# Performance work log

Hardware: AMD Instinct MI355X
Metric: run time of the kernel (lower is better)

## Reference

```python
import jax, jax.numpy as jnp
import numpy as np

N = 100000
E = 1600000
DIM = 64
HEADS = 8
HEAD_DIM = DIM // HEADS
LN_EPS = 1e-5
NORM_EPS = 1e-12


def setup_inputs() -> dict:
    key = jax.random.key(0)
    ks = jax.random.split(key, 5)
    x = jax.random.normal(ks[0], (N, DIM), dtype=jnp.float32)
    edge_index = jax.random.randint(ks[1], (2, E), 0, N, dtype=jnp.int32)
    W_w = jax.random.normal(ks[2], (DIM, DIM), dtype=jnp.float32) * (1.0 / np.sqrt(DIM))
    W_b = jax.random.normal(ks[3], (DIM,), dtype=jnp.float32) * 0.01
    a = jax.random.normal(ks[4], (HEADS, 2 * HEAD_DIM), dtype=jnp.float32) * 0.1
    ln_scale = jnp.ones((DIM,), dtype=jnp.float32)
    ln_bias = jnp.zeros((DIM,), dtype=jnp.float32)
    return {"x": x, "edge_index": edge_index, "W_w": W_w, "W_b": W_b,
            "a": a, "ln_scale": ln_scale, "ln_bias": ln_bias}


def reference(x, edge_index, W_w, W_b, a, ln_scale, ln_bias):
    n = x.shape[0]
    # Linear (dropout = identity in eval), reshape to heads
    h = (x @ W_w.T + W_b).reshape(n, HEADS, HEAD_DIM)          # [N,H,D]
    src, dst = edge_index[0], edge_index[1]
    hs = h[src]                                                 # [E,H,D]
    hd = h[dst]                                                 # [E,H,D]
    a_src, a_dst = a[:, :HEAD_DIM], a[:, HEAD_DIM:]             # [H,D] each
    # (a * cat(hs, hd)).sum(-1) split over the two halves
    alpha = jnp.einsum('ehd,hd->eh', hs, a_src) + jnp.einsum('ehd,hd->eh', hd, a_dst)
    alpha = jnp.where(alpha >= 0, alpha, 0.2 * alpha)           # LeakyReLU(0.2)
    alpha = jax.nn.softmax(alpha, axis=1)                       # NOTE: over heads, as in source
    msg = alpha[..., None] * hd                                 # [E,H,D]
    out = jax.ops.segment_sum(msg, src, num_segments=n)         # scatter-add to src nodes
    out = out.reshape(n, DIM)
    # residual + LayerNorm
    y = out + x
    mu = jnp.mean(y, axis=-1, keepdims=True)
    var = jnp.mean((y - mu) ** 2, axis=-1, keepdims=True)
    y = (y - mu) * jax.lax.rsqrt(var + LN_EPS) * ln_scale + ln_bias
    # F.normalize(p=2, dim=-1)
    norm = jnp.sqrt(jnp.sum(y * y, axis=-1, keepdims=True))
    return y / jnp.maximum(norm, NORM_EPS)
```

## Files before the change

kernel.cpp:

```cpp
#include <hip/hip_runtime.h>
#include <hip/hip_fp16.h>
#include <math.h>

#define N_NODES 100000
#define N_EDGES 1600000
#define LN_EPS 1e-5f
#define NORM_EPS 1e-12f
#define ROWS_PER_BLOCK 32
#define GEMM_BLOCKS (N_NODES / ROWS_PER_BLOCK)
#define WSTRIDE 66
#define WB 64
#define NBKT ((N_NODES + WB - 1) / WB)
#define BIN_TILE 8192
#define BIN_BLOCKS ((N_EDGES + BIN_TILE - 1) / BIN_TILE)

__global__ __launch_bounds__(256) void k_gemm(
    const float* __restrict__ x, const float* __restrict__ W,
    const float* __restrict__ b, const float* __restrict__ a,
    __half* __restrict__ h16,
    float* __restrict__ s_src, float* __restrict__ s_dst)
{
    __shared__ float WL[64 * WSTRIDE];
    __shared__ float xs[ROWS_PER_BLOCK * 64];
    const int tid  = threadIdx.x;
    const int lane = tid & 63;
    const int wv   = tid >> 6;

    for (int idx = tid * 4; idx < 64 * 64; idx += 256 * 4) {
        const float4 w = *(const float4*)(W + idx);
        const int c = idx >> 6, k = idx & 63;
        WL[c * WSTRIDE + k + 0] = w.x;
        WL[c * WSTRIDE + k + 1] = w.y;
        WL[c * WSTRIDE + k + 2] = w.z;
        WL[c * WSTRIDE + k + 3] = w.w;
    }
    const int row0 = blockIdx.x * ROWS_PER_BLOCK;
    for (int idx = tid * 4; idx < ROWS_PER_BLOCK * 64; idx += 256 * 4)
        *(float4*)(xs + idx) = *(const float4*)(x + (size_t)row0 * 64 + idx);
    __syncthreads();

    const float bias = b[lane];
    float acc[8];
    #pragma unroll
    for (int r = 0; r < 8; ++r) acc[r] = bias;

    const int rbase = wv * 8;
    const float* wrow = WL + lane * WSTRIDE;
    const float* xrow = xs + rbase * 64;
    #pragma unroll 1
    for (int kk = 0; kk < 64; kk += 4) {
        const float2 w01 = *(const float2*)(wrow + kk);
        const float2 w23 = *(const float2*)(wrow + kk + 2);
        #pragma unroll
        for (int r = 0; r < 8; ++r) {
            const float4 xq = *(const float4*)(xrow + r * 64 + kk);
            acc[r] += xq.x * w01.x + xq.y * w01.y + xq.z * w23.x + xq.w * w23.y;
        }
    }

    const float asrc = a[(lane >> 3) * 16 + (lane & 7)];
    const float adst = a[(lane >> 3) * 16 + 8 + (lane & 7)];
    #pragma unroll
    for (int r = 0; r < 8; ++r) {
        const int row = row0 + rbase + r;
        const float v = acc[r];
        h16[(size_t)row * 64 + lane] = __float2half_rn(v);
        float p = v * asrc, q = v * adst;
        p += __shfl_xor(p, 1);  q += __shfl_xor(q, 1);
        p += __shfl_xor(p, 2);  q += __shfl_xor(q, 2);
        p += __shfl_xor(p, 4);  q += __shfl_xor(q, 4);
        if ((lane & 7) == 0) {
            s_src[row * 8 + (lane >> 3)] = p;
            s_dst[row * 8 + (lane >> 3)] = q;
        }
    }
}

__global__ __launch_bounds__(1024) void k_hist(
    const int* __restrict__ ei, int* __restrict__ bhist)
{
    __shared__ int hist[NBKT];
    const int tid = threadIdx.x;
    for (int b = tid; b < NBKT; b += 1024) hist[b] = 0;
    __syncthreads();
    const int e0 = blockIdx.x * BIN_TILE;
    #pragma unroll
    for (int j = 0; j < 8; ++j) {
        const int e = e0 + j * 1024 + tid;
        if (e < N_EDGES) atomicAdd(&hist[ei[e] >> 6], 1);
    }
    __syncthreads();
    for (int b = tid; b < NBKT; b += 1024)
        if (hist[b]) atomicAdd(&bhist[b], hist[b]);
}

__global__ __launch_bounds__(1024) void k_bscan(
    const int* __restrict__ bhist, int* __restrict__ bucket_base,
    int* __restrict__ gbin)
{
    __shared__ int wsum[16];
    const int tid = threadIdx.x, lane = tid & 63, wv = tid >> 6;

    int v = (tid < NBKT) ? bhist[tid] : 0;
    int sc = v;
    #pragma unroll
    for (int off = 1; off < 64; off <<= 1) {
        int t = __shfl_up(sc, off);
        if (lane >= off) sc += t;
    }
    if (lane == 63) wsum[wv] = sc;
    __syncthreads();
    if (tid < 16) {
        int ws = wsum[tid];
        #pragma unroll
        for (int off = 1; off < 16; off <<= 1) {
            int t = __shfl_up(ws, off);
            if (tid >= off) ws += t;
        }
        wsum[tid] = ws;
    }
    __syncthreads();
    const int pref0 = wv ? wsum[wv - 1] : 0;
    const int ex0 = pref0 + sc - v;
    if (tid < NBKT) { bucket_base[tid] = ex0; gbin[tid] = ex0; }
    const int T1 = wsum[15];
    __syncthreads();

    const int i2 = 1024 + tid;
    int v2 = (i2 < NBKT) ? bhist[i2] : 0;
    int sc2 = v2;
    #pragma unroll
    for (int off = 1; off < 64; off <<= 1) {
        int t = __shfl_up(sc2, off);
        if (lane >= off) sc2 += t;
    }
    if (lane == 63) wsum[wv] = sc2;
    __syncthreads();
    if (tid < 16) {
        int ws = wsum[tid];
        #pragma unroll
        for (int off = 1; off < 16; off <<= 1) {
            int t = __shfl_up(ws, off);
            if (tid >= off) ws += t;
        }
        wsum[tid] = ws;
    }
    __syncthreads();
    const int pref1 = wv ? wsum[wv - 1] : 0;
    const int ex1 = T1 + pref1 + sc2 - v2;
    if (i2 < NBKT) { bucket_base[i2] = ex1; gbin[i2] = ex1; }
    if (tid == 0) bucket_base[NBKT] = N_EDGES;
}

__global__ __launch_bounds__(1024) void k_bin(
    const int* __restrict__ ei, int* __restrict__ gbin,
    unsigned int* __restrict__ staged)
{
    __shared__ int hist[NBKT];
    __shared__ int base[NBKT];
    const int tid = threadIdx.x;
    for (int b = tid; b < NBKT; b += 1024) hist[b] = 0;
    __syncthreads();

    int s[8], d[8], r[8];
    const int e0 = blockIdx.x * BIN_TILE;
    #pragma unroll
    for (int j = 0; j < 8; ++j) {
        const int e = e0 + j * 1024 + tid;
        if (e < N_EDGES) {
            s[j] = ei[e];
            d[j] = ei[N_EDGES + e];
            r[j] = atomicAdd(&hist[s[j] >> 6], 1);
        }
    }
    __syncthreads();
    for (int b = tid; b < NBKT; b += 1024)
        if (hist[b]) base[b] = atomicAdd(&gbin[b], hist[b]);
    __syncthreads();
    #pragma unroll
    for (int j = 0; j < 8; ++j) {
        const int e = e0 + j * 1024 + tid;
        if (e < N_EDGES)
            staged[(size_t)base[s[j] >> 6] + r[j]] =
                (unsigned int)((s[j] & 63) | (d[j] << 6));
    }
}

__global__ __launch_bounds__(1024) void k_place(
    const int* __restrict__ bucket_base, const unsigned int* __restrict__ staged,
    const float* __restrict__ s_src, const float* __restrict__ s_dst,
    int* __restrict__ row_ptr, int* __restrict__ dst_sorted,
    __half* __restrict__ alpha16)
{
    __shared__ int cnt[WB];
    __shared__ int cur[WB];
    const int g   = blockIdx.x;
    const int n0  = g * WB;
    const int tid = threadIdx.x;
    if (tid < WB) cnt[tid] = 0;
    __syncthreads();
    const int beg = bucket_base[g];
    const int end = bucket_base[g + 1];

    for (int j = beg + tid; j < end; j += 1024)
        atomicAdd(&cnt[staged[j] & 63u], 1);
    __syncthreads();
    if (tid < WB) {
        const int c = cnt[tid];
        int sc = c;
        #pragma unroll
        for (int off = 1; off < 64; off <<= 1) {
            int t = __shfl_up(sc, off);
            if (tid >= off) sc += t;
        }
        const int rp = beg + sc - c;
        cur[tid] = rp;
        if (n0 + tid < N_NODES) row_ptr[n0 + tid] = rp;
    }
    if (g == NBKT - 1 && tid == 0) row_ptr[N_NODES] = N_EDGES;
    __syncthreads();

    for (int j = beg + tid; j < end; j += 1024) {
        const unsigned int w = staged[j];
        const int srcl = (int)(w & 63u);
        const int dst  = (int)(w >> 6);

        const float4 a0 = *(const float4*)(s_src + (size_t)(n0 + srcl) * 8);
        const float4 a1 = *(const float4*)(s_src + (size_t)(n0 + srcl) * 8 + 4);
        const float4 b0 = *(const float4*)(s_dst + (size_t)dst * 8);
        const float4 b1 = *(const float4*)(s_dst + (size_t)dst * 8 + 4);
        float sc[8] = {a0.x + b0.x, a0.y + b0.y, a0.z + b0.z, a0.w + b0.w,
                       a1.x + b1.x, a1.y + b1.y, a1.z + b1.z, a1.w + b1.w};
        float m = -1e30f;
        #pragma unroll
        for (int h = 0; h < 8; ++h) {
            sc[h] = (sc[h] >= 0.f) ? sc[h] : 0.2f * sc[h];
            m = fmaxf(m, sc[h]);
        }
        float sum = 0.f;
        #pragma unroll
        for (int h = 0; h < 8; ++h) { sc[h] = __expf(sc[h] - m); sum += sc[h]; }
        const float inv = 1.f / sum;
        unsigned int q[4];
        #pragma unroll
        for (int jj = 0; jj < 4; ++jj) {
            const unsigned short lo = __half_as_ushort(__float2half_rn(sc[2*jj]   * inv));
            const unsigned short hi = __half_as_ushort(__float2half_rn(sc[2*jj+1] * inv));
            q[jj] = (unsigned int)lo | ((unsigned int)hi << 16);
        }

        const int slot = atomicAdd(&cur[srcl], 1);
        dst_sorted[slot] = dst;
        *(uint4*)(alpha16 + (size_t)slot * 8) = make_uint4(q[0], q[1], q[2], q[3]);
    }
}

__global__ __launch_bounds__(256) void k_gather(
    const int* __restrict__ row_ptr, const int* __restrict__ dst_sorted,
    const __half* __restrict__ alpha16, const __half* __restrict__ h16,
    const float* __restrict__ x, const float* __restrict__ ln_scale,
    const float* __restrict__ ln_bias, float* __restrict__ out)
{
    const int i = __builtin_amdgcn_readfirstlane(
        blockIdx.x * 4 + (threadIdx.x >> 6));
    if (i >= N_NODES) return;
    const int lane = threadIdx.x & 63;
    const int head = lane >> 3;

    const int beg = row_ptr[i];
    const int end = row_ptr[i + 1];
    const float xres = x[(size_t)i * 64 + lane];

    float acc = 0.f;
    int e = beg;
    for (; e + 7 < end; e += 8) {
        int d[8];
        #pragma unroll
        for (int j = 0; j < 8; ++j) d[j] = dst_sorted[e + j];
        float al[8];
        #pragma unroll
        for (int j = 0; j < 8; ++j)
            al[j] = __half2float(alpha16[(size_t)(e + j) * 8 + head]);
        float hv[8];
        #pragma unroll
        for (int j = 0; j < 8; ++j)
            hv[j] = __half2float(h16[(size_t)d[j] * 64 + lane]);
        #pragma unroll
        for (int j = 0; j < 8; ++j) acc = fmaf(al[j], hv[j], acc);
    }
    for (; e + 3 < end; e += 4) {
        int d[4];
        #pragma unroll
        for (int j = 0; j < 4; ++j) d[j] = dst_sorted[e + j];
        float al[4];
        #pragma unroll
        for (int j = 0; j < 4; ++j)
            al[j] = __half2float(alpha16[(size_t)(e + j) * 8 + head]);
        float hv[4];
        #pragma unroll
        for (int j = 0; j < 4; ++j)
            hv[j] = __half2float(h16[(size_t)d[j] * 64 + lane]);
        #pragma unroll
        for (int j = 0; j < 4; ++j) acc = fmaf(al[j], hv[j], acc);
    }
    for (; e < end; ++e)
        acc = fmaf(__half2float(alpha16[(size_t)e * 8 + head]),
                   __half2float(h16[(size_t)dst_sorted[e] * 64 + lane]), acc);

    float v = acc + xres;
    float s = v;
    #pragma unroll
    for (int off = 1; off < 64; off <<= 1) s += __shfl_xor(s, off);
    const float mu = s * (1.f / 64.f);
    const float d = v - mu;
    float vs = d * d;
    #pragma unroll
    for (int off = 1; off < 64; off <<= 1) vs += __shfl_xor(vs, off);
    const float var = vs * (1.f / 64.f);
    float y = d * rsqrtf(var + LN_EPS) * ln_scale[lane] + ln_bias[lane];
    float ss = y * y;
    #pragma unroll
    for (int off = 1; off < 64; off <<= 1) ss += __shfl_xor(ss, off);
    const float norm = sqrtf(ss);
    out[(size_t)i * 64 + lane] = y / fmaxf(norm, NORM_EPS);
}

extern "C" void kernel_launch(void* const* d_in, const int* in_sizes, int n_in,
                              void* d_out, int out_size, void* d_ws, size_t ws_size,
                              hipStream_t stream)
{
    const float* x        = (const float*)d_in[0];
    const int*   ei       = (const int*)d_in[1];
    const float* W        = (const float*)d_in[2];
    const float* b        = (const float*)d_in[3];
    const float* a        = (const float*)d_in[4];
    const float* ln_scale = (const float*)d_in[5];
    const float* ln_bias  = (const float*)d_in[6];
    float* out = (float*)d_out;

    char* ws = (char*)d_ws;
    size_t off = 0;
    auto alloc = [&](size_t bytes) {
        void* p = ws + off;
        off = (off + bytes + 255) & ~(size_t)255;
        return p;
    };
    __half* h16        = (__half*)alloc((size_t)N_NODES * 64 * 2);
    float*  s_src      = (float*) alloc((size_t)N_NODES * 8 * 4);
    float*  s_dst      = (float*) alloc((size_t)N_NODES * 8 * 4);
    int*    bhist      = (int*)   alloc((size_t)NBKT * 4);
    int*    bucket_base= (int*)   alloc((size_t)(NBKT + 1) * 4);
    int*    gbin       = (int*)   alloc((size_t)NBKT * 4);
    int*    row_ptr    = (int*)   alloc((size_t)(N_NODES + 1) * 4);
    unsigned int* staged = (unsigned int*)alloc((size_t)N_EDGES * 4);
    int*    dst_sorted = (int*)   alloc((size_t)N_EDGES * 4);
    __half* alpha16    = (__half*)alloc((size_t)N_EDGES * 8 * 2);

    hipMemsetAsync(bhist, 0, (size_t)NBKT * 4, stream);

    k_hist  <<<BIN_BLOCKS, 1024, 0, stream>>>(ei, bhist);
    k_bscan <<<1, 1024, 0, stream>>>(bhist, bucket_base, gbin);
    k_gemm  <<<GEMM_BLOCKS, 256, 0, stream>>>(x, W, b, a, h16, s_src, s_dst);
    k_bin   <<<BIN_BLOCKS, 1024, 0, stream>>>(ei, gbin, staged);
    k_place <<<NBKT, 1024, 0, stream>>>(bucket_base, staged, s_src, s_dst,
                                        row_ptr, dst_sorted, alpha16);
    k_gather<<<(N_NODES + 3) / 4, 256, 0, stream>>>(row_ptr, dst_sorted, alpha16,
                                                    h16, x, ln_scale, ln_bias, out);
}
```

Measured before the change: 226.4 us.

## Merge edge binning into GEMM kernel as a heterogeneous block grid

Folds the edge-binning kernel into the node GEMM kernel so one launch runs both: the first BIN2_BLOCKS blocks do binning with 256 threads over 2048-edge tiles, and the rest do the GEMM. Dynamic shared memory is sized to hold either the bin histogram and base arrays or the GEMM's W and x tiles. This removes one kernel launch and its serialization boundary, letting independent binning and GEMM work share the GPU. In exchange the binning tiles are four times smaller, so there are more global atomics on gbin, and shared-memory use per block rises to the larger of the two roles.

```diff
diff --git a/kernel.cpp b/kernel.cpp
--- a/kernel.cpp
+++ b/kernel.cpp
@@ -13,16 +13,54 @@
 #define NBKT ((N_NODES + WB - 1) / WB)
 #define BIN_TILE 8192
 #define BIN_BLOCKS ((N_EDGES + BIN_TILE - 1) / BIN_TILE)
-
-__global__ __launch_bounds__(256) void k_gemm(
+#define BIN2_TILE 2048
+#define BIN2_BLOCKS ((N_EDGES + BIN2_TILE - 1) / BIN2_TILE)
+#define GB_LDS 25088
+
+__global__ __launch_bounds__(256) void k_gemm_bin(
     const float* __restrict__ x, const float* __restrict__ W,
     const float* __restrict__ b, const float* __restrict__ a,
     __half* __restrict__ h16,
-    float* __restrict__ s_src, float* __restrict__ s_dst)
-{
-    __shared__ float WL[64 * WSTRIDE];
-    __shared__ float xs[ROWS_PER_BLOCK * 64];
-    const int tid  = threadIdx.x;
+    float* __restrict__ s_src, float* __restrict__ s_dst,
+    const int* __restrict__ ei, int* __restrict__ gbin,
+    unsigned int* __restrict__ staged)
+{
+    extern __shared__ char smem[];
+    const int tid = threadIdx.x;
+
+    if (blockIdx.x < BIN2_BLOCKS) {
+        int* hist = (int*)smem;
+        int* base = hist + NBKT;
+        for (int bb = tid; bb < NBKT; bb += 256) hist[bb] = 0;
+        __syncthreads();
+
+        int s[8], d[8], r[8];
+        const int e0 = blockIdx.x * BIN2_TILE;
+        #pragma unroll
+        for (int j = 0; j < 8; ++j) {
+            const int e = e0 + j * 256 + tid;
+            if (e < N_EDGES) {
+                s[j] = ei[e];
+                d[j] = ei[N_EDGES + e];
+                r[j] = atomicAdd(&hist[s[j] >> 6], 1);
+            }
+        }
+        __syncthreads();
+        for (int bb = tid; bb < NBKT; bb += 256)
+            if (hist[bb]) base[bb] = atomicAdd(&gbin[bb], hist[bb]);
+        __syncthreads();
+        #pragma unroll
+        for (int j = 0; j < 8; ++j) {
+            const int e = e0 + j * 256 + tid;
+            if (e < N_EDGES)
+                staged[(size_t)base[s[j] >> 6] + r[j]] =
+                    (unsigned int)((s[j] & 63) | (d[j] << 6));
+        }
+        return;
+    }
+
+    float* WL = (float*)smem;
+    float* xs = WL + 64 * WSTRIDE;
     const int lane = tid & 63;
     const int wv   = tid >> 6;
 
@@ -34,7 +72,7 @@
         WL[c * WSTRIDE + k + 2] = w.z;
         WL[c * WSTRIDE + k + 3] = w.w;
     }
-    const int row0 = blockIdx.x * ROWS_PER_BLOCK;
+    const int row0 = (blockIdx.x - BIN2_BLOCKS) * ROWS_PER_BLOCK;
     for (int idx = tid * 4; idx < ROWS_PER_BLOCK * 64; idx += 256 * 4)
         *(float4*)(xs + idx) = *(const float4*)(x + (size_t)row0 * 64 + idx);
     __syncthreads();
@@ -150,40 +188,6 @@
     const int ex1 = T1 + pref1 + sc2 - v2;
     if (i2 < NBKT) { bucket_base[i2] = ex1; gbin[i2] = ex1; }
     if (tid == 0) bucket_base[NBKT] = N_EDGES;
-}
-
-__global__ __launch_bounds__(1024) void k_bin(
-    const int* __restrict__ ei, int* __restrict__ gbin,
-    unsigned int* __restrict__ staged)
-{
-    __shared__ int hist[NBKT];
-    __shared__ int base[NBKT];
-    const int tid = threadIdx.x;
-    for (int b = tid; b < NBKT; b += 1024) hist[b] = 0;
-    __syncthreads();
-
-    int s[8], d[8], r[8];
-    const int e0 = blockIdx.x * BIN_TILE;
-    #pragma unroll
-    for (int j = 0; j < 8; ++j) {
-        const int e = e0 + j * 1024 + tid;
-        if (e < N_EDGES) {
-            s[j] = ei[e];
-            d[j] = ei[N_EDGES + e];
-            r[j] = atomicAdd(&hist[s[j] >> 6], 1);
-        }
-    }
-    __syncthreads();
-    for (int b = tid; b < NBKT; b += 1024)
-        if (hist[b]) base[b] = atomicAdd(&gbin[b], hist[b]);
-    __syncthreads();
-    #pragma unroll
-    for (int j = 0; j < 8; ++j) {
-        const int e = e0 + j * 1024 + tid;
-        if (e < N_EDGES)
-            staged[(size_t)base[s[j] >> 6] + r[j]] =
-                (unsigned int)((s[j] & 63) | (d[j] << 6));
-    }
 }
 
 __global__ __launch_bounds__(1024) void k_place(
@@ -358,12 +362,12 @@
 
     hipMemsetAsync(bhist, 0, (size_t)NBKT * 4, stream);
 
-    k_hist  <<<BIN_BLOCKS, 1024, 0, stream>>>(ei, bhist);
-    k_bscan <<<1, 1024, 0, stream>>>(bhist, bucket_base, gbin);
-    k_gemm  <<<GEMM_BLOCKS, 256, 0, stream>>>(x, W, b, a, h16, s_src, s_dst);
-    k_bin   <<<BIN_BLOCKS, 1024, 0, stream>>>(ei, gbin, staged);
-    k_place <<<NBKT, 1024, 0, stream>>>(bucket_base, staged, s_src, s_dst,
-                                        row_ptr, dst_sorted, alpha16);
-    k_gather<<<(N_NODES + 3) / 4, 256, 0, stream>>>(row_ptr, dst_sorted, alpha16,
-                                                    h16, x, ln_scale, ln_bias, out);
-}
+    k_hist    <<<BIN_BLOCKS, 1024, 0, stream>>>(ei, bhist);
+    k_bscan   <<<1, 1024, 0, stream>>>(bhist, bucket_base, gbin);
+    k_gemm_bin<<<BIN2_BLOCKS + GEMM_BLOCKS, 256, GB_LDS, stream>>>(
+        x, W, b, a, h16, s_src, s_dst, ei, gbin, staged);
+    k_place   <<<NBKT, 1024, 0, stream>>>(bucket_base, staged, s_src, s_dst,
+                                          row_ptr, dst_sorted, alpha16);
+    k_gather  <<<(N_NODES + 3) / 4, 256, 0, stream>>>(row_ptr, dst_sorted, alpha16,
+                                                      h16, x, ln_scale, ln_bias, out);
+}
```

After: 237.8 us. 1.05x slower.
